# Optimization experiments

Hardware: AMD Instinct MI355X
Metric: run time of the kernel (lower is better)

The kernel has to match this reference:

```python
import jax, jax.numpy as jnp
import numpy as np

S = 7
B = 2
C = 20
LAMBDA_COORD = 5.0
LAMBDA_NOOBJ = 0.5
EPS = 1e-6
N_IMG = 8192
N_GT = 32


def setup_inputs() -> dict:
    key = jax.random.key(0)
    k1, k2, k3 = jax.random.split(key, 3)
    outputs = jax.random.uniform(k1, (N_IMG, S, S, B * 5 + C), dtype=jnp.float32)
    gt_boxes = jax.random.uniform(k2, (N_IMG, N_GT, 4), dtype=jnp.float32)
    gt_labels = jax.random.randint(k3, (N_IMG, N_GT), 0, C)
    return {"outputs": outputs, "gt_boxes": gt_boxes, "gt_labels": gt_labels}


def _pairwise_iou(pred, gt):
    # pred: [N,S,S,B,1,4], gt: [N,1,1,1,G,4], boxes in (cx, cy, w, h) format
    px1 = pred[..., 0] - pred[..., 2] * 0.5
    py1 = pred[..., 1] - pred[..., 3] * 0.5
    px2 = pred[..., 0] + pred[..., 2] * 0.5
    py2 = pred[..., 1] + pred[..., 3] * 0.5
    gx1 = gt[..., 0] - gt[..., 2] * 0.5
    gy1 = gt[..., 1] - gt[..., 3] * 0.5
    gx2 = gt[..., 0] + gt[..., 2] * 0.5
    gy2 = gt[..., 1] + gt[..., 3] * 0.5
    iw = jnp.clip(jnp.minimum(px2, gx2) - jnp.maximum(px1, gx1), 0.0)
    ih = jnp.clip(jnp.minimum(py2, gy2) - jnp.maximum(py1, gy1), 0.0)
    inter = iw * ih
    union = pred[..., 2] * pred[..., 3] + gt[..., 2] * gt[..., 3] - inter
    return inter / (union + EPS)  # [N,S,S,B,G]


def reference(outputs, gt_boxes, gt_labels):
    N = outputs.shape[0]
    pb = outputs[..., : B * 5].reshape(N, S, S, B, 5)
    pbox = pb[..., :4]          # [N,S,S,B,4]
    pconf = pb[..., 4]          # [N,S,S,B]
    pcls = outputs[..., B * 5:] # [N,S,S,C]

    iou = _pairwise_iou(pbox[:, :, :, :, None, :], gt_boxes[:, None, None, None, :, :])
    best_iou = iou.max(axis=-1)      # [N,S,S,B]
    best_idx = iou.argmax(axis=-1)   # [N,S,S,B]

    # gather matched GT boxes: [N,S,S,B,4]
    matched = jnp.take_along_axis(
        gt_boxes[:, None, None, None, :, :], best_idx[..., None, None], axis=4
    ).squeeze(4)

    loc = LAMBDA_COORD * (
        (pbox[..., 0] - matched[..., 0]) ** 2
        + (pbox[..., 1] - matched[..., 1]) ** 2
        + (jnp.sqrt(pbox[..., 2]) - jnp.sqrt(matched[..., 2])) ** 2
        + (jnp.sqrt(pbox[..., 3]) - jnp.sqrt(matched[..., 3])) ** 2
    )
    conf_obj = (pconf - best_iou) ** 2

    # multi-hot class target per image (scatter 1 at every GT label)
    multihot = jnp.zeros((N, C), outputs.dtype).at[
        jnp.arange(N)[:, None], gt_labels
    ].set(1.0)
    # soft-target cross entropy: -sum(t * log_softmax(logits)) per cell
    ce = -(jax.nn.log_softmax(pcls, axis=-1) * multihot[:, None, None, :]).sum(-1)  # [N,S,S]

    has_obj = best_iou > 0.0
    per_box = jnp.where(has_obj, loc + conf_obj + ce[..., None], LAMBDA_NOOBJ * pconf ** 2)
    return per_box.sum() / N
```

## Files before the change

kernel.cpp:

```cpp
#include <hip/hip_runtime.h>

#define NC 20
#define NCELL 49
#define NGT 32
#define NIMG 8192
#define NTOT (NIMG * NCELL)
#define CPB 128
#define NTILE (NTOT / CPB)
#define PBLK 1024
#define NSPAN 4
#define LAMBDA_COORD 5.0f
#define LAMBDA_NOOBJ 0.5f
#define EPS_IOU 1e-6f

__global__ __launch_bounds__(256, 4) void yolo_main_kernel(
    const float* __restrict__ outputs,
    const float* __restrict__ gt_boxes,
    const int*   __restrict__ gt_labels,
    float* __restrict__ partials)
{
    __shared__ float4   s_act4[2][CPB * 30 / 4];
    __shared__ float4   s_gtc[2][NSPAN * NGT];
    __shared__ float    s_ga [2][NSPAN * NGT];
    __shared__ unsigned s_mask[2][NSPAN];
    __shared__ float    s_w[4];

    const int tid = threadIdx.x;
    const int bid = blockIdx.x;
    const int nt  = 3 + (bid < (NTILE - 3 * PBLK) ? 1 : 0);

    float acc = 0.f;

    float4 r0, r1, r2, r3, gtr;
    unsigned labbit = 0u;
    unsigned g_img = NIMG;

#define STAGE_ISSUE(base_) do {                                               \
    const float4* asrc_ = reinterpret_cast<const float4*>(outputs)            \
                        + (size_t)(base_) * 30 / 4;                           \
    r0 = asrc_[tid];                                                          \
    r1 = asrc_[tid + 256];                                                    \
    r2 = asrc_[tid + 512];                                                    \
    if (tid < 192) r3 = asrc_[tid + 768];                                     \
    const unsigned il_ = (base_) / NCELL;                                     \
    if (tid < 128) {                                                          \
        const unsigned g_ = (unsigned)tid >> 5;                               \
        g_img = il_ + g_;                                                     \
        if (g_img < NIMG)                                                     \
            gtr = reinterpret_cast<const float4*>(gt_boxes)[g_img * NGT + (tid & 31)]; \
    } else {                                                                  \
        const int t_ = tid - 128;                                             \
        const unsigned g_ = (unsigned)t_ >> 5;                                \
        g_img = il_ + g_;                                                     \
        labbit = (g_img < NIMG) ? (1u << gt_labels[g_img * NGT + (t_ & 31)])  \
                                : 0u;                                         \
    }                                                                         \
} while (0)

#define STAGE_WRITE(nb_) do {                                                 \
    s_act4[nb_][tid]       = r0;                                              \
    s_act4[nb_][tid + 256] = r1;                                              \
    s_act4[nb_][tid + 512] = r2;                                              \
    if (tid < 192) s_act4[nb_][tid + 768] = r3;                               \
    if (tid < 128) {                                                          \
        if (g_img < NIMG) {                                                   \
            s_gtc[nb_][tid] = make_float4(fmaf(gtr.z, -0.5f, gtr.x),          \
                                          fmaf(gtr.w, -0.5f, gtr.y),          \
                                          fmaf(gtr.z,  0.5f, gtr.x),          \
                                          fmaf(gtr.w,  0.5f, gtr.y));         \
            s_ga[nb_][tid] = gtr.z * gtr.w;                                   \
        }                                                                     \
    } else {                                                                  \
        unsigned m_ = labbit;                                                 \
        m_ |= __shfl_xor(m_, 1, 32);                                          \
        m_ |= __shfl_xor(m_, 2, 32);                                          \
        m_ |= __shfl_xor(m_, 4, 32);                                          \
        m_ |= __shfl_xor(m_, 8, 32);                                          \
        m_ |= __shfl_xor(m_, 16, 32);                                         \
        const int t_ = tid - 128;                                             \
        if ((t_ & 31) == 0) s_mask[nb_][t_ >> 5] = m_;                        \
    }                                                                         \
} while (0)

    STAGE_ISSUE((unsigned)bid * CPB);
    STAGE_WRITE(0);
    __syncthreads();

    int cur = 0;
    for (int k = 0; k < nt; ++k) {
        const unsigned tile = (unsigned)bid + (unsigned)k * PBLK;
        const unsigned base = tile * CPB;
        const bool hn = (k + 1 < nt);
        if (hn) STAGE_ISSUE((tile + PBLK) * CPB);

        const unsigned img_lo = base / NCELL;
        const unsigned off    = base - img_lo * NCELL;

        const int p = tid & 1;
        const int s = tid >> 1;
        const unsigned rel  = ((unsigned)(s + off) * 1339u) >> 16;
        const unsigned mask = s_mask[cur][rel];
        const float2* a2 = reinterpret_cast<const float2*>(s_act4[cur]) + s * 15;

        const float2* cp = a2 + 5 + p * 5;
        float2 c0 = cp[0], c1 = cp[1], c2 = cp[2], c3 = cp[3], c4 = cp[4];
        float mxh = fmaxf(fmaxf(fmaxf(c0.x, c0.y), fmaxf(c1.x, c1.y)),
                          fmaxf(fmaxf(c2.x, c2.y), fmaxf(c3.x, c3.y)));
        mxh = fmaxf(mxh, fmaxf(c4.x, c4.y));
        const unsigned mh = mask >> (p * 10);
        float selh = ((mh & 1u)   ? c0.x : 0.f) + ((mh & 2u)   ? c0.y : 0.f)
                   + ((mh & 4u)   ? c1.x : 0.f) + ((mh & 8u)   ? c1.y : 0.f)
                   + ((mh & 16u)  ? c2.x : 0.f) + ((mh & 32u)  ? c2.y : 0.f)
                   + ((mh & 64u)  ? c3.x : 0.f) + ((mh & 128u) ? c3.y : 0.f)
                   + ((mh & 256u) ? c4.x : 0.f) + ((mh & 512u) ? c4.y : 0.f);
        const float mx = fmaxf(mxh, __shfl_xor(mxh, 1));
        float ssh = __expf(c0.x - mx) + __expf(c0.y - mx)
                  + __expf(c1.x - mx) + __expf(c1.y - mx)
                  + __expf(c2.x - mx) + __expf(c2.y - mx)
                  + __expf(c3.x - mx) + __expf(c3.y - mx)
                  + __expf(c4.x - mx) + __expf(c4.y - mx);
        const float ssum = ssh + __shfl_xor(ssh, 1);
        const float sel  = selh + __shfl_xor(selh, 1);
        const float ce = (float)__popc(mask) * (mx + __logf(ssum)) - sel;

        float2 A = a2[2 * p], Bv = a2[2 * p + 1], Cv = a2[2 * p + 2];
        const float cx = p ? A.y  : A.x;
        const float cy = p ? Bv.x : A.y;
        const float w  = p ? Bv.y : Bv.x;
        const float h  = p ? Cv.x : Bv.y;
        const float cf = p ? Cv.y : Cv.x;

        const float px1 = fmaf(w, -0.5f, cx), py1 = fmaf(h, -0.5f, cy);
        const float px2 = fmaf(w,  0.5f, cx), py2 = fmaf(h,  0.5f, cy);
        const float pae = w * h + EPS_IOU;

        const float4* gtc = s_gtc[cur] + rel * NGT;
        const float*  gab = s_ga[cur]  + rel * NGT;
        float bin = -1.f, bS = 1.f;
        int bi = 0;
        #pragma unroll
        for (int j = 0; j < NGT; j += 2) {
            float4 g0 = gtc[j], g1 = gtc[j + 1];
            float2 ar = *reinterpret_cast<const float2*>(gab + j);
            {
                float iw = fmaxf(fminf(px2, g0.z) - fmaxf(px1, g0.x), 0.f);
                float ih = fmaxf(fminf(py2, g0.w) - fmaxf(py1, g0.y), 0.f);
                float in = iw * ih, S = pae + ar.x;
                if (in * bS > bin * S) { bin = in; bS = S; bi = j; }
            }
            {
                float iw = fmaxf(fminf(px2, g1.z) - fmaxf(px1, g1.x), 0.f);
                float ih = fmaxf(fminf(py2, g1.w) - fmaxf(py1, g1.y), 0.f);
                float in = iw * ih, S = pae + ar.y;
                if (in * bS > bin * S) { bin = in; bS = S; bi = j + 1; }
            }
        }

        float term;
        if (bin > 0.f) {
            float4 g = gtc[bi];
            const float iou = __fdividef(bin, bS - bin);
            const float dx = cx - (g.x + g.z) * 0.5f;
            const float dy = cy - (g.y + g.w) * 0.5f;
            const float dw = sqrtf(w) - sqrtf(g.z - g.x);
            const float dh = sqrtf(h) - sqrtf(g.w - g.y);
            term = LAMBDA_COORD * (dx * dx + dy * dy + dw * dw + dh * dh)
                 + (cf - iou) * (cf - iou) + ce;
        } else {
            term = LAMBDA_NOOBJ * cf * cf;
        }
        acc += term;

        if (hn) STAGE_WRITE(cur ^ 1);
        __syncthreads();
        cur ^= 1;
    }

    #pragma unroll
    for (int o = 32; o > 0; o >>= 1)
        acc += __shfl_down(acc, o);
    if ((tid & 63) == 0) s_w[tid >> 6] = acc;
    __syncthreads();
    if (tid == 0)
        partials[bid] = s_w[0] + s_w[1] + s_w[2] + s_w[3];
}

__global__ __launch_bounds__(256) void yolo_reduce_kernel(
    const float* __restrict__ partials, float* __restrict__ out)
{
    float s = 0.f;
    #pragma unroll
    for (int k = 0; k < PBLK / 256; ++k)
        s += partials[threadIdx.x + k * 256];
    #pragma unroll
    for (int o = 32; o > 0; o >>= 1)
        s += __shfl_down(s, o);
    __shared__ float s_w[4];
    const int tid = threadIdx.x;
    if ((tid & 63) == 0) s_w[tid >> 6] = s;
    __syncthreads();
    if (tid == 0)
        out[0] = (s_w[0] + s_w[1] + s_w[2] + s_w[3]) * (1.0f / (float)NIMG);
}

extern "C" void kernel_launch(void* const* d_in, const int* in_sizes, int n_in,
                              void* d_out, int out_size, void* d_ws, size_t ws_size,
                              hipStream_t stream) {
    const float* outputs   = (const float*)d_in[0];
    const float* gt_boxes  = (const float*)d_in[1];
    const int*   gt_labels = (const int*)d_in[2];
    float* out      = (float*)d_out;
    float* partials = (float*)d_ws;

    yolo_main_kernel<<<PBLK, 256, 0, stream>>>(outputs, gt_boxes, gt_labels, partials);
    yolo_reduce_kernel<<<1, 256, 0, stream>>>(partials, out);
}
```

Baseline: 28.65 us.

## Restructure main kernel to process one image per tile with 128-thread blocks

Each block iteration now stages exactly one image (49 cells, 32 GT boxes, one label mask) instead of a 128-cell tile that straddles up to four images. This removes the per-cell image-index division, the redundant multi-image GT and label staging, and the span lookup. The cost is that only 98 of 128 threads do work per tile, and activations are loaded as float2 rather than float4. Grid size doubles and block size halves, with four images per block in a double-buffered loop.

```diff
diff --git a/kernel.cpp b/kernel.cpp
--- a/kernel.cpp
+++ b/kernel.cpp
@@ -4,172 +4,157 @@
 #define NCELL 49
 #define NGT 32
 #define NIMG 8192
-#define NTOT (NIMG * NCELL)
-#define CPB 128
-#define NTILE (NTOT / CPB)
-#define PBLK 1024
-#define NSPAN 4
+#define PBLK 2048
+#define TPB 4
 #define LAMBDA_COORD 5.0f
 #define LAMBDA_NOOBJ 0.5f
 #define EPS_IOU 1e-6f
 
-__global__ __launch_bounds__(256, 4) void yolo_main_kernel(
+__global__ __launch_bounds__(128, 4) void yolo_main_kernel(
     const float* __restrict__ outputs,
     const float* __restrict__ gt_boxes,
     const int*   __restrict__ gt_labels,
     float* __restrict__ partials)
 {
-    __shared__ float4   s_act4[2][CPB * 30 / 4];
-    __shared__ float4   s_gtc[2][NSPAN * NGT];
-    __shared__ float    s_ga [2][NSPAN * NGT];
-    __shared__ unsigned s_mask[2][NSPAN];
-    __shared__ float    s_w[4];
+    __shared__ float2   s_act[2][736];
+    __shared__ float4   s_gtc[2][NGT];
+    __shared__ float    s_ga [2][NGT];
+    __shared__ unsigned s_mask[2];
+    __shared__ float    s_w[2];
 
     const int tid = threadIdx.x;
     const int bid = blockIdx.x;
-    const int nt  = 3 + (bid < (NTILE - 3 * PBLK) ? 1 : 0);
 
     float acc = 0.f;
 
-    float4 r0, r1, r2, r3, gtr;
+    float2 r0, r1, r2, r3, r4, r5;
+    float4 gtr;
     unsigned labbit = 0u;
-    unsigned g_img = NIMG;
-
-#define STAGE_ISSUE(base_) do {                                               \
-    const float4* asrc_ = reinterpret_cast<const float4*>(outputs)            \
-                        + (size_t)(base_) * 30 / 4;                           \
-    r0 = asrc_[tid];                                                          \
-    r1 = asrc_[tid + 256];                                                    \
-    r2 = asrc_[tid + 512];                                                    \
-    if (tid < 192) r3 = asrc_[tid + 768];                                     \
-    const unsigned il_ = (base_) / NCELL;                                     \
-    if (tid < 128) {                                                          \
-        const unsigned g_ = (unsigned)tid >> 5;                               \
-        g_img = il_ + g_;                                                     \
-        if (g_img < NIMG)                                                     \
-            gtr = reinterpret_cast<const float4*>(gt_boxes)[g_img * NGT + (tid & 31)]; \
-    } else {                                                                  \
-        const int t_ = tid - 128;                                             \
-        const unsigned g_ = (unsigned)t_ >> 5;                                \
-        g_img = il_ + g_;                                                     \
-        labbit = (g_img < NIMG) ? (1u << gt_labels[g_img * NGT + (t_ & 31)])  \
-                                : 0u;                                         \
-    }                                                                         \
+
+#define STAGE_ISSUE(img_) do {                                                \
+    const float2* src_ = reinterpret_cast<const float2*>(outputs)             \
+                       + (size_t)(img_) * 735;                                \
+    r0 = src_[tid];                                                           \
+    r1 = src_[tid + 128];                                                     \
+    r2 = src_[tid + 256];                                                     \
+    r3 = src_[tid + 384];                                                     \
+    r4 = src_[tid + 512];                                                     \
+    if (tid < 95) r5 = src_[tid + 640];                                       \
+    if (tid < 32)                                                             \
+        gtr = reinterpret_cast<const float4*>(gt_boxes)[(img_) * NGT + tid];  \
+    else if (tid < 64)                                                        \
+        labbit = 1u << gt_labels[(img_) * NGT + (tid - 32)];                  \
 } while (0)
 
 #define STAGE_WRITE(nb_) do {                                                 \
-    s_act4[nb_][tid]       = r0;                                              \
-    s_act4[nb_][tid + 256] = r1;                                              \
-    s_act4[nb_][tid + 512] = r2;                                              \
-    if (tid < 192) s_act4[nb_][tid + 768] = r3;                               \
-    if (tid < 128) {                                                          \
-        if (g_img < NIMG) {                                                   \
-            s_gtc[nb_][tid] = make_float4(fmaf(gtr.z, -0.5f, gtr.x),          \
-                                          fmaf(gtr.w, -0.5f, gtr.y),          \
-                                          fmaf(gtr.z,  0.5f, gtr.x),          \
-                                          fmaf(gtr.w,  0.5f, gtr.y));         \
-            s_ga[nb_][tid] = gtr.z * gtr.w;                                   \
-        }                                                                     \
-    } else {                                                                  \
+    s_act[nb_][tid]       = r0;                                               \
+    s_act[nb_][tid + 128] = r1;                                               \
+    s_act[nb_][tid + 256] = r2;                                               \
+    s_act[nb_][tid + 384] = r3;                                               \
+    s_act[nb_][tid + 512] = r4;                                               \
+    if (tid < 95) s_act[nb_][tid + 640] = r5;                                 \
+    if (tid < 32) {                                                           \
+        s_gtc[nb_][tid] = make_float4(fmaf(gtr.z, -0.5f, gtr.x),              \
+                                      fmaf(gtr.w, -0.5f, gtr.y),              \
+                                      fmaf(gtr.z,  0.5f, gtr.x),              \
+                                      fmaf(gtr.w,  0.5f, gtr.y));             \
+        s_ga[nb_][tid] = gtr.z * gtr.w;                                       \
+    } else if (tid < 64) {                                                    \
         unsigned m_ = labbit;                                                 \
         m_ |= __shfl_xor(m_, 1, 32);                                          \
         m_ |= __shfl_xor(m_, 2, 32);                                          \
         m_ |= __shfl_xor(m_, 4, 32);                                          \
         m_ |= __shfl_xor(m_, 8, 32);                                          \
         m_ |= __shfl_xor(m_, 16, 32);                                         \
-        const int t_ = tid - 128;                                             \
-        if ((t_ & 31) == 0) s_mask[nb_][t_ >> 5] = m_;                        \
+        if (tid == 32) s_mask[nb_] = m_;                                      \
     }                                                                         \
 } while (0)
 
-    STAGE_ISSUE((unsigned)bid * CPB);
+    STAGE_ISSUE(bid);
     STAGE_WRITE(0);
     __syncthreads();
 
     int cur = 0;
-    for (int k = 0; k < nt; ++k) {
-        const unsigned tile = (unsigned)bid + (unsigned)k * PBLK;
-        const unsigned base = tile * CPB;
-        const bool hn = (k + 1 < nt);
-        if (hn) STAGE_ISSUE((tile + PBLK) * CPB);
-
-        const unsigned img_lo = base / NCELL;
-        const unsigned off    = base - img_lo * NCELL;
-
-        const int p = tid & 1;
-        const int s = tid >> 1;
-        const unsigned rel  = ((unsigned)(s + off) * 1339u) >> 16;
-        const unsigned mask = s_mask[cur][rel];
-        const float2* a2 = reinterpret_cast<const float2*>(s_act4[cur]) + s * 15;
-
-        const float2* cp = a2 + 5 + p * 5;
-        float2 c0 = cp[0], c1 = cp[1], c2 = cp[2], c3 = cp[3], c4 = cp[4];
-        float mxh = fmaxf(fmaxf(fmaxf(c0.x, c0.y), fmaxf(c1.x, c1.y)),
-                          fmaxf(fmaxf(c2.x, c2.y), fmaxf(c3.x, c3.y)));
-        mxh = fmaxf(mxh, fmaxf(c4.x, c4.y));
-        const unsigned mh = mask >> (p * 10);
-        float selh = ((mh & 1u)   ? c0.x : 0.f) + ((mh & 2u)   ? c0.y : 0.f)
-                   + ((mh & 4u)   ? c1.x : 0.f) + ((mh & 8u)   ? c1.y : 0.f)
-                   + ((mh & 16u)  ? c2.x : 0.f) + ((mh & 32u)  ? c2.y : 0.f)
-                   + ((mh & 64u)  ? c3.x : 0.f) + ((mh & 128u) ? c3.y : 0.f)
-                   + ((mh & 256u) ? c4.x : 0.f) + ((mh & 512u) ? c4.y : 0.f);
-        const float mx = fmaxf(mxh, __shfl_xor(mxh, 1));
-        float ssh = __expf(c0.x - mx) + __expf(c0.y - mx)
-                  + __expf(c1.x - mx) + __expf(c1.y - mx)
-                  + __expf(c2.x - mx) + __expf(c2.y - mx)
-                  + __expf(c3.x - mx) + __expf(c3.y - mx)
-                  + __expf(c4.x - mx) + __expf(c4.y - mx);
-        const float ssum = ssh + __shfl_xor(ssh, 1);
-        const float sel  = selh + __shfl_xor(selh, 1);
-        const float ce = (float)__popc(mask) * (mx + __logf(ssum)) - sel;
-
-        float2 A = a2[2 * p], Bv = a2[2 * p + 1], Cv = a2[2 * p + 2];
-        const float cx = p ? A.y  : A.x;
-        const float cy = p ? Bv.x : A.y;
-        const float w  = p ? Bv.y : Bv.x;
-        const float h  = p ? Cv.x : Bv.y;
-        const float cf = p ? Cv.y : Cv.x;
-
-        const float px1 = fmaf(w, -0.5f, cx), py1 = fmaf(h, -0.5f, cy);
-        const float px2 = fmaf(w,  0.5f, cx), py2 = fmaf(h,  0.5f, cy);
-        const float pae = w * h + EPS_IOU;
-
-        const float4* gtc = s_gtc[cur] + rel * NGT;
-        const float*  gab = s_ga[cur]  + rel * NGT;
-        float bin = -1.f, bS = 1.f;
-        int bi = 0;
-        #pragma unroll
-        for (int j = 0; j < NGT; j += 2) {
-            float4 g0 = gtc[j], g1 = gtc[j + 1];
-            float2 ar = *reinterpret_cast<const float2*>(gab + j);
-            {
-                float iw = fmaxf(fminf(px2, g0.z) - fmaxf(px1, g0.x), 0.f);
-                float ih = fmaxf(fminf(py2, g0.w) - fmaxf(py1, g0.y), 0.f);
-                float in = iw * ih, S = pae + ar.x;
-                if (in * bS > bin * S) { bin = in; bS = S; bi = j; }
+    #pragma unroll 1
+    for (int k = 0; k < TPB; ++k) {
+        const bool hn = (k + 1 < TPB);
+        if (hn) STAGE_ISSUE(bid + (k + 1) * PBLK);
+
+        if (tid < 2 * NCELL) {
+            const unsigned mask = s_mask[cur];
+            const int p = tid & 1;
+            const int s = tid >> 1;
+            const float2* a2 = s_act[cur] + s * 15;
+
+            const float2* cp = a2 + 5 + p * 5;
+            float2 c0 = cp[0], c1 = cp[1], c2 = cp[2], c3 = cp[3], c4 = cp[4];
+            float mxh = fmaxf(fmaxf(fmaxf(c0.x, c0.y), fmaxf(c1.x, c1.y)),
+                              fmaxf(fmaxf(c2.x, c2.y), fmaxf(c3.x, c3.y)));
+            mxh = fmaxf(mxh, fmaxf(c4.x, c4.y));
+            const unsigned mh = mask >> (p * 10);
+            float selh = ((mh & 1u)   ? c0.x : 0.f) + ((mh & 2u)   ? c0.y : 0.f)
+                       + ((mh & 4u)   ? c1.x : 0.f) + ((mh & 8u)   ? c1.y : 0.f)
+                       + ((mh & 16u)  ? c2.x : 0.f) + ((mh & 32u)  ? c2.y : 0.f)
+                       + ((mh & 64u)  ? c3.x : 0.f) + ((mh & 128u) ? c3.y : 0.f)
+                       + ((mh & 256u) ? c4.x : 0.f) + ((mh & 512u) ? c4.y : 0.f);
+            const float mx = fmaxf(mxh, __shfl_xor(mxh, 1));
+            float ssh = __expf(c0.x - mx) + __expf(c0.y - mx)
+                      + __expf(c1.x - mx) + __expf(c1.y - mx)
+                      + __expf(c2.x - mx) + __expf(c2.y - mx)
+                      + __expf(c3.x - mx) + __expf(c3.y - mx)
+                      + __expf(c4.x - mx) + __expf(c4.y - mx);
+            const float ssum = ssh + __shfl_xor(ssh, 1);
+            const float sel  = selh + __shfl_xor(selh, 1);
+            const float ce = (float)__popc(mask) * (mx + __logf(ssum)) - sel;
+
+            float2 A = a2[2 * p], Bv = a2[2 * p + 1], Cv = a2[2 * p + 2];
+            const float cx = p ? A.y  : A.x;
+            const float cy = p ? Bv.x : A.y;
+            const float w  = p ? Bv.y : Bv.x;
+            const float h  = p ? Cv.x : Bv.y;
+            const float cf = p ? Cv.y : Cv.x;
+
+            const float px1 = fmaf(w, -0.5f, cx), py1 = fmaf(h, -0.5f, cy);
+            const float px2 = fmaf(w,  0.5f, cx), py2 = fmaf(h,  0.5f, cy);
+            const float pae = w * h + EPS_IOU;
+
+            const float4* gtc = s_gtc[cur];
+            const float*  gab = s_ga[cur];
+            float bin = -1.f, bS = 1.f;
+            int bi = 0;
+            #pragma unroll
+            for (int j = 0; j < NGT; j += 2) {
+                float4 g0 = gtc[j], g1 = gtc[j + 1];
+                float2 ar = *reinterpret_cast<const float2*>(gab + j);
+                {
+                    float iw = fmaxf(fminf(px2, g0.z) - fmaxf(px1, g0.x), 0.f);
+                    float ih = fmaxf(fminf(py2, g0.w) - fmaxf(py1, g0.y), 0.f);
+                    float in = iw * ih, S = pae + ar.x;
+                    if (in * bS > bin * S) { bin = in; bS = S; bi = j; }
+                }
+                {
+                    float iw = fmaxf(fminf(px2, g1.z) - fmaxf(px1, g1.x), 0.f);
+                    float ih = fmaxf(fminf(py2, g1.w) - fmaxf(py1, g1.y), 0.f);
+                    float in = iw * ih, S = pae + ar.y;
+                    if (in * bS > bin * S) { bin = in; bS = S; bi = j + 1; }
+                }
             }
-            {
-                float iw = fmaxf(fminf(px2, g1.z) - fmaxf(px1, g1.x), 0.f);
-                float ih = fmaxf(fminf(py2, g1.w) - fmaxf(py1, g1.y), 0.f);
-                float in = iw * ih, S = pae + ar.y;
-                if (in * bS > bin * S) { bin = in; bS = S; bi = j + 1; }
+
+            float term;
+            if (bin > 0.f) {
+                float4 g = gtc[bi];
+                const float iou = __fdividef(bin, bS - bin);
+                const float dx = cx - (g.x + g.z) * 0.5f;
+                const float dy = cy - (g.y + g.w) * 0.5f;
+                const float dw = sqrtf(w) - sqrtf(g.z - g.x);
+                const float dh = sqrtf(h) - sqrtf(g.w - g.y);
+                term = LAMBDA_COORD * (dx * dx + dy * dy + dw * dw + dh * dh)
+                     + (cf - iou) * (cf - iou) + ce;
+            } else {
+                term = LAMBDA_NOOBJ * cf * cf;
             }
+            acc += term;
         }
-
-        float term;
-        if (bin > 0.f) {
-            float4 g = gtc[bi];
-            const float iou = __fdividef(bin, bS - bin);
-            const float dx = cx - (g.x + g.z) * 0.5f;
-            const float dy = cy - (g.y + g.w) * 0.5f;
-            const float dw = sqrtf(w) - sqrtf(g.z - g.x);
-            const float dh = sqrtf(h) - sqrtf(g.w - g.y);
-            term = LAMBDA_COORD * (dx * dx + dy * dy + dw * dw + dh * dh)
-                 + (cf - iou) * (cf - iou) + ce;
-        } else {
-            term = LAMBDA_NOOBJ * cf * cf;
-        }
-        acc += term;
 
         if (hn) STAGE_WRITE(cur ^ 1);
         __syncthreads();
@@ -182,7 +167,7 @@
     if ((tid & 63) == 0) s_w[tid >> 6] = acc;
     __syncthreads();
     if (tid == 0)
-        partials[bid] = s_w[0] + s_w[1] + s_w[2] + s_w[3];
+        partials[bid] = s_w[0] + s_w[1];
 }
 
 __global__ __launch_bounds__(256) void yolo_reduce_kernel(
@@ -212,6 +197,6 @@
     float* out      = (float*)d_out;
     float* partials = (float*)d_ws;
 
-    yolo_main_kernel<<<PBLK, 256, 0, stream>>>(outputs, gt_boxes, gt_labels, partials);
+    yolo_main_kernel<<<PBLK, 128, 0, stream>>>(outputs, gt_boxes, gt_labels, partials);
     yolo_reduce_kernel<<<1, 256, 0, stream>>>(partials, out);
 }
```

Result: slower. 32.76 us (+14.4%).
